# Kernel tuning notes

Measured on AMD Instinct MI355X. Metric: run time of the kernel, lower is better.

The kernel has to match this reference:

```python
import jax, jax.numpy as jnp
import numpy as np

B, N, TOKEN_DIM = 8, 1024, 768
H, D = 12, 64  # n_heads, head_dim


def setup_inputs() -> dict:
    key = jax.random.key(0)
    k1, k2, k3, k4 = jax.random.split(key, 4)
    x = jax.random.normal(k1, (B, N, TOKEN_DIM), dtype=jnp.float32)
    # nn.Linear(token_dim, 3*H*D, bias=False); store as (in, out)
    W_qkv = jax.random.normal(k2, (TOKEN_DIM, 3 * H * D), dtype=jnp.float32) * (TOKEN_DIM ** -0.5)
    # nn.Linear(H*D, token_dim) with bias
    W_out = jax.random.normal(k3, (H * D, TOKEN_DIM), dtype=jnp.float32) * ((H * D) ** -0.5)
    b_out = jax.random.normal(k4, (TOKEN_DIM,), dtype=jnp.float32) * 0.01
    return {"x": x, "W_qkv": W_qkv, "W_out": W_out, "b_out": b_out}


def reference(x, W_qkv, W_out, b_out):
    b, n, _ = x.shape
    qkv = x @ W_qkv                              # (B, N, 3*H*D)
    # Faithful to original: reshape directly to (B, 3, H, N, D)
    qkv = qkv.reshape(b, 3, H, n, D)
    q, k, v = qkv[:, 0], qkv[:, 1], qkv[:, 2]    # each (B, H, N, D)
    scale = D ** -0.5
    scores = jnp.einsum('bhnd,bhmd->bhnm', q, k) * scale
    probs = jax.nn.softmax(scores, axis=-1)
    attn = jnp.einsum('bhnm,bhmd->bhnd', probs, v)  # (B, H, N, D)
    attn = attn.transpose(0, 2, 1, 3).reshape(b, n, H * D)
    out = attn @ W_out + b_out                    # dropout p=0.0 is identity
    return out
```

## Files before the change

### kernel.cpp

```cpp
#include <hip/hip_runtime.h>
#include <math.h>

static constexpr int NB   = 8;
static constexpr int SEQ  = 1024;
static constexpr int TD   = 768;
static constexpr int NH   = 12;
static constexpr int HD   = 64;
static constexpr int QKVC = 3 * NH * HD;

static constexpr size_t BATCH_ELEMS = (size_t)SEQ * QKVC;
static constexpr size_t THIRD_ELEMS = (size_t)NH * SEQ * HD;
static constexpr size_t HEAD_ELEMS  = (size_t)SEQ * HD;

typedef __bf16 bf16x8 __attribute__((ext_vector_type(8)));
typedef __bf16 bf16x4 __attribute__((ext_vector_type(4)));
typedef float  f32x4  __attribute__((ext_vector_type(4)));

#define MFMA16(a, b, c) __builtin_amdgcn_mfma_f32_16x16x32_bf16((a), (b), (c), 0, 0, 0)

static constexpr float SCL2E = 0.18033688011112042f;

__device__ __forceinline__ void gload_lds16(const void* g, void* l) {
  __builtin_amdgcn_global_load_lds(
      (const __attribute__((address_space(1))) unsigned int*)g,
      (__attribute__((address_space(3))) unsigned int*)l, 16, 0, 0);
}

__global__ __launch_bounds__(256) void cast_f32_bf16(const float* __restrict__ in,
                                                     __bf16* __restrict__ out, int n4) {
  int i = blockIdx.x * 256 + threadIdx.x;
  if (i < n4) {
    float4 v = ((const float4*)in)[i];
    bf16x4 o;
    o[0] = (__bf16)v.x; o[1] = (__bf16)v.y; o[2] = (__bf16)v.z; o[3] = (__bf16)v.w;
    ((bf16x4*)out)[i] = o;
  }
}

__global__ __launch_bounds__(256) void wtrans(const float* __restrict__ W,
                                              __bf16* __restrict__ Wt, int K, int N) {
  __shared__ float T[32 * 33];
  const int tid = threadIdx.x;
  const int k0 = blockIdx.y * 32, n0 = blockIdx.x * 32;
#pragma unroll
  for (int i = 0; i < 4; ++i) {
    int idx = tid + i * 256;
    int kk = idx >> 5, nn = idx & 31;
    T[kk * 33 + nn] = W[(size_t)(k0 + kk) * N + n0 + nn];
  }
  __syncthreads();
#pragma unroll
  for (int i = 0; i < 4; ++i) {
    int idx = tid + i * 256;
    int nn = idx >> 5, kk = idx & 31;
    Wt[(size_t)(n0 + nn) * K + k0 + kk] = (__bf16)T[kk * 33 + nn];
  }
}

__global__ __launch_bounds__(256) void vtrans(const __bf16* __restrict__ qkvb,
                                              __bf16* __restrict__ vtb) {
  const int nt = blockIdx.x;
  const int h = blockIdx.y;
  const int b = blockIdx.z;
  __shared__ __bf16 T[128 * 72];
  const int tid = threadIdx.x;
  const int n0 = nt * 128;
  const __bf16* Vb = qkvb + (size_t)b * BATCH_ELEMS + 2 * THIRD_ELEMS + (size_t)h * HEAD_ELEMS;
#pragma unroll
  for (int i = 0; i < 4; ++i) {
    int ch = tid + i * 256;
    int row = ch >> 3, c8 = ch & 7;
    *(bf16x8*)&T[row * 72 + c8 * 8] = *(const bf16x8*)&Vb[(size_t)(n0 + row) * HD + c8 * 8];
  }
  __syncthreads();
#pragma unroll
  for (int i = 0; i < 4; ++i) {
    int ch = tid + i * 256;
    int d = ch >> 4, n8 = ch & 15;
    bf16x8 v;
#pragma unroll
    for (int jj = 0; jj < 8; ++jj) {
      int j = (jj + n8) & 7;
      v[j] = T[(n8 * 8 + j) * 72 + d];
    }
    *(bf16x8*)&vtb[((size_t)((b * NH + h) * HD) + d) * SEQ + n0 + n8 * 8] = v;
  }
}

template <int MODE, int BM>
__global__ __launch_bounds__(256) void gemm_mfma(const __bf16* __restrict__ A,
                                                 const __bf16* __restrict__ Bt,
                                                 const float* __restrict__ bias,
                                                 void* __restrict__ C,
                                                 int M, int N, int K) {
  constexpr int MI = BM / 32;
  __shared__ __bf16 As[2][BM * 32];
  __shared__ __bf16 Bs[2][128 * 32];
  const int tid = threadIdx.x;
  const int lane = tid & 63;
  const int wid = tid >> 6;
  const int wr = wid >> 1, wc = wid & 1;
  const int r = lane & 15, g = lane >> 4;
  const size_t bm = (size_t)blockIdx.y * BM;
  const size_t bn = (size_t)blockIdx.x * 128;

  const int srow = lane >> 2;
  const int scol = (lane & 3) * 8;

  auto stage = [&](int buf, int k0) {
#pragma unroll
    for (int j = 0; j < BM / 64; ++j) {
      const int rowbase = wid * (BM / 4) + j * 16;
      gload_lds16(&A[(bm + rowbase + srow) * K + k0 + scol], &As[buf][rowbase * 32]);
    }
#pragma unroll
    for (int j = 0; j < 2; ++j) {
      const int rowbase = wid * 32 + j * 16;
      gload_lds16(&Bt[(bn + rowbase + srow) * K + k0 + scol], &Bs[buf][rowbase * 32]);
    }
  };

  f32x4 acc[MI][4];
#pragma unroll
  for (int mi = 0; mi < MI; ++mi)
#pragma unroll
    for (int nj = 0; nj < 4; ++nj) acc[mi][nj] = (f32x4){0.f, 0.f, 0.f, 0.f};

  stage(0, 0);
  __syncthreads();

  int cur = 0;
  for (int k0 = 0; k0 < K; k0 += 32) {
    if (k0 + 32 < K) stage(cur ^ 1, k0 + 32);
    bf16x8 af[MI], bf[4];
#pragma unroll
    for (int mi = 0; mi < MI; ++mi)
      af[mi] = *(const bf16x8*)&As[cur][(wr * (BM / 2) + mi * 16 + r) * 32 + g * 8];
#pragma unroll
    for (int nj = 0; nj < 4; ++nj)
      bf[nj] = *(const bf16x8*)&Bs[cur][(wc * 64 + nj * 16 + r) * 32 + g * 8];
    __builtin_amdgcn_s_setprio(1);
#pragma unroll
    for (int mi = 0; mi < MI; ++mi)
#pragma unroll
      for (int nj = 0; nj < 4; ++nj)
        acc[mi][nj] = MFMA16(af[mi], bf[nj], acc[mi][nj]);
    __builtin_amdgcn_s_setprio(0);
    __syncthreads();
    cur ^= 1;
  }

  const int orow0 = g * 4;
  const int ocol = r;
#pragma unroll
  for (int mi = 0; mi < MI; ++mi)
#pragma unroll
    for (int nj = 0; nj < 4; ++nj)
#pragma unroll
      for (int reg = 0; reg < 4; ++reg) {
        size_t rrow = bm + wr * (BM / 2) + mi * 16 + orow0 + reg;
        size_t ccol = bn + wc * 64 + nj * 16 + ocol;
        float v = acc[mi][nj][reg];
        if (MODE == 1) {
          int fwb = ((int)(rrow & (SEQ - 1))) * QKVC + (int)ccol;
          float vv = (fwb < (int)THIRD_ELEMS) ? v * SCL2E : v;
          ((__bf16*)C)[rrow * N + ccol] = (__bf16)vv;
        } else {
          ((float*)C)[rrow * N + ccol] = v + bias[ccol];
        }
      }
}

__global__ __launch_bounds__(256) void attn_mfma(const __bf16* __restrict__ qkvb,
                                                 const __bf16* __restrict__ vtb,
                                                 __bf16* __restrict__ attn2b) {
  const int d = blockIdx.x;
  const int qt = (d >> 3) & 7;
  const int hb = (d >> 6) * 8 + (d & 7);
  const int b = hb / NH, h = hb % NH;

  const int tid = threadIdx.x;
  const int lane = tid & 63;
  const int w = tid >> 6;
  const int c = lane & 15, g = lane >> 4;

  __shared__ __bf16 KsF[2][4096];
  __shared__ __bf16 VsF[2][4096];

  const __bf16* Qb = qkvb + (size_t)b * BATCH_ELEMS + (size_t)h * HEAD_ELEMS;
  const __bf16* Kb = Qb + THIRD_ELEMS;
  const __bf16* Vtb = vtb + (size_t)((b * NH + h) * HD) * SEQ;

  const __bf16* kS[2];
  const __bf16* vS[2];
  int ldsOff[2];
#pragma unroll
  for (int i = 0; i < 2; ++i) {
    const int t2f = i * 4 + w;
    const int t = t2f >> 1, f = t2f & 1;
    const int krow = ((t >> 1) << 5) | ((c >> 2) << 3) | ((t & 1) << 2) | (c & 3);
    kS[i] = Kb + krow * HD + f * 32 + g * 8;
    const int db = t2f >> 1, kk = t2f & 1;
    vS[i] = Vtb + (db * 16 + c) * SEQ + kk * 32 + g * 8;
    ldsOff[i] = t2f * 512;
  }

  bf16x8 qf[2][2];
#pragma unroll
  for (int s = 0; s < 2; ++s) {
    const int q0s = qt * 128 + s * 64 + w * 16;
#pragma unroll
    for (int f = 0; f < 2; ++f)
      qf[s][f] = *(const bf16x8*)&Qb[(size_t)(q0s + c) * HD + f * 32 + g * 8];
  }

  f32x4 Oa[2][4];
#pragma unroll
  for (int s = 0; s < 2; ++s)
#pragma unroll
    for (int db = 0; db < 4; ++db) Oa[s][db] = (f32x4){0.f, 0.f, 0.f, 0.f};
  float lpart[2] = {0.f, 0.f};

#pragma unroll
  for (int i = 0; i < 2; ++i) {
    gload_lds16(kS[i], &KsF[0][ldsOff[i]]);
    gload_lds16(vS[i], &VsF[0][ldsOff[i]]);
    kS[i] += 64 * HD;
    vS[i] += 64;
  }
  __syncthreads();

  int cur = 0;
  for (int it = 0; it < SEQ / 64; ++it) {
    if (it < SEQ / 64 - 1) {
      const int nxt = cur ^ 1;
#pragma unroll
      for (int i = 0; i < 2; ++i) {
        gload_lds16(kS[i], &KsF[nxt][ldsOff[i]]);
        gload_lds16(vS[i], &VsF[nxt][ldsOff[i]]);
        kS[i] += 64 * HD;
        vS[i] += 64;
      }
    }

    f32x4 sa[2][4];
#pragma unroll
    for (int s = 0; s < 2; ++s)
#pragma unroll
      for (int t = 0; t < 4; ++t) sa[s][t] = (f32x4){0.f, 0.f, 0.f, 0.f};
    __builtin_amdgcn_s_setprio(1);
#pragma unroll
    for (int t = 0; t < 4; ++t)
#pragma unroll
      for (int f = 0; f < 2; ++f) {
        bf16x8 kf = *(const bf16x8*)&KsF[cur][(t * 2 + f) * 512 + lane * 8];
        sa[0][t] = MFMA16(kf, qf[0][f], sa[0][t]);
        sa[1][t] = MFMA16(kf, qf[1][f], sa[1][t]);
      }
    __builtin_amdgcn_s_setprio(0);

    bf16x8 pb[2][2];
#pragma unroll
    for (int s = 0; s < 2; ++s) {
      float p[4][4];
      float lp = 0.f;
#pragma unroll
      for (int t = 0; t < 4; ++t)
#pragma unroll
        for (int reg = 0; reg < 4; ++reg) {
          float pv = __builtin_exp2f(sa[s][t][reg]);
          p[t][reg] = pv;
          lp += pv;
        }
      lpart[s] += lp;
#pragma unroll
      for (int kk = 0; kk < 2; ++kk)
#pragma unroll
        for (int i = 0; i < 4; ++i) {
          pb[s][kk][i] = (__bf16)p[2 * kk][i];
          pb[s][kk][4 + i] = (__bf16)p[2 * kk + 1][i];
        }
    }

    __builtin_amdgcn_s_setprio(1);
#pragma unroll
    for (int db = 0; db < 4; ++db)
#pragma unroll
      for (int kk = 0; kk < 2; ++kk) {
        bf16x8 vf = *(const bf16x8*)&VsF[cur][(db * 2 + kk) * 512 + lane * 8];
        Oa[0][db] = MFMA16(vf, pb[0][kk], Oa[0][db]);
        Oa[1][db] = MFMA16(vf, pb[1][kk], Oa[1][db]);
      }
    __builtin_amdgcn_s_setprio(0);

    __syncthreads();
    cur ^= 1;
  }

#pragma unroll
  for (int s = 0; s < 2; ++s) {
    float lrow = lpart[s];
    lrow += __shfl_xor(lrow, 16);
    lrow += __shfl_xor(lrow, 32);
    const float inv = 1.0f / lrow;
    const size_t rowq = (size_t)(b * SEQ) + qt * 128 + s * 64 + w * 16 + c;
#pragma unroll
    for (int db = 0; db < 4; ++db) {
      bf16x4 o;
#pragma unroll
      for (int reg = 0; reg < 4; ++reg) o[reg] = (__bf16)(Oa[s][db][reg] * inv);
      *(bf16x4*)&attn2b[rowq * TD + h * HD + db * 16 + g * 4] = o;
    }
  }
}

extern "C" void kernel_launch(void* const* d_in, const int* in_sizes, int n_in,
                              void* d_out, int out_size, void* d_ws,
                              size_t ws_size, hipStream_t stream) {
  const float* x = (const float*)d_in[0];
  const float* W_qkv = (const float*)d_in[1];
  const float* W_out = (const float*)d_in[2];
  const float* b_out = (const float*)d_in[3];
  float* out = (float*)d_out;

  __bf16* xb = (__bf16*)d_ws;
  __bf16* wqkvt = xb + (size_t)NB * SEQ * TD;
  __bf16* woutt = wqkvt + (size_t)QKVC * TD;
  __bf16* qkvb = woutt + (size_t)TD * TD;
  __bf16* vtb = qkvb + (size_t)NB * SEQ * QKVC;
  __bf16* attn2b = vtb + (size_t)NB * NH * HD * SEQ;

  cast_f32_bf16<<<(NB * SEQ * TD / 4 + 255) / 256, 256, 0, stream>>>(x, xb, NB * SEQ * TD / 4);
  wtrans<<<dim3(QKVC / 32, TD / 32), 256, 0, stream>>>(W_qkv, wqkvt, TD, QKVC);
  wtrans<<<dim3(TD / 32, TD / 32), 256, 0, stream>>>(W_out, woutt, TD, TD);

  gemm_mfma<1, 128><<<dim3(QKVC / 128, NB * SEQ / 128), 256, 0, stream>>>(
      xb, wqkvt, nullptr, qkvb, NB * SEQ, QKVC, TD);

  vtrans<<<dim3(SEQ / 128, NH, NB), 256, 0, stream>>>(qkvb, vtb);

  attn_mfma<<<dim3(SEQ / 128 * NH * NB), 256, 0, stream>>>(qkvb, vtb, attn2b);

  gemm_mfma<0, 64><<<dim3(TD / 128, NB * SEQ / 64), 256, 0, stream>>>(
      attn2b, woutt, b_out, out, NB * SEQ, TD, TD);
}
```

Baseline: 153.3 us.

## Load attention K/V fragments directly from global into registers, drop LDS staging

The attention kernel no longer stages K and V tiles through double-buffered shared memory with async global-to-LDS loads and per-iteration barriers. Each wave now loads its MFMA fragments for K and V straight from global memory into registers every iteration, and the loop is kept rolled. The setprio hints around MFMA blocks are also removed in both the GEMM and attention kernels. This removes LDS traffic and __syncthreads, but every wave now re-reads the same K/V data from global/L2 and loses the prefetch overlap, so it depends on cache hits and latency hiding.

```diff
diff --git a/kernel.cpp b/kernel.cpp
--- a/kernel.cpp
+++ b/kernel.cpp
@@ -139,13 +139,11 @@
 #pragma unroll
     for (int nj = 0; nj < 4; ++nj)
       bf[nj] = *(const bf16x8*)&Bs[cur][(wc * 64 + nj * 16 + r) * 32 + g * 8];
-    __builtin_amdgcn_s_setprio(1);
 #pragma unroll
     for (int mi = 0; mi < MI; ++mi)
 #pragma unroll
       for (int nj = 0; nj < 4; ++nj)
         acc[mi][nj] = MFMA16(af[mi], bf[nj], acc[mi][nj]);
-    __builtin_amdgcn_s_setprio(0);
     __syncthreads();
     cur ^= 1;
   }
@@ -184,26 +182,16 @@
   const int w = tid >> 6;
   const int c = lane & 15, g = lane >> 4;
 
-  __shared__ __bf16 KsF[2][4096];
-  __shared__ __bf16 VsF[2][4096];
-
   const __bf16* Qb = qkvb + (size_t)b * BATCH_ELEMS + (size_t)h * HEAD_ELEMS;
   const __bf16* Kb = Qb + THIRD_ELEMS;
   const __bf16* Vtb = vtb + (size_t)((b * NH + h) * HD) * SEQ;
 
-  const __bf16* kS[2];
-  const __bf16* vS[2];
-  int ldsOff[2];
-#pragma unroll
-  for (int i = 0; i < 2; ++i) {
-    const int t2f = i * 4 + w;
-    const int t = t2f >> 1, f = t2f & 1;
-    const int krow = ((t >> 1) << 5) | ((c >> 2) << 3) | ((t & 1) << 2) | (c & 3);
-    kS[i] = Kb + krow * HD + f * 32 + g * 8;
-    const int db = t2f >> 1, kk = t2f & 1;
-    vS[i] = Vtb + (db * 16 + c) * SEQ + kk * 32 + g * 8;
-    ldsOff[i] = t2f * 512;
-  }
+  const __bf16* kb0 = Kb + ((c >> 2) * 8 + (c & 3)) * HD + g * 8;
+  const __bf16* kb1 = kb0 + 2048;
+  const __bf16* vb0 = Vtb + (size_t)(0 * 16 + c) * SEQ + g * 8;
+  const __bf16* vb1 = Vtb + (size_t)(1 * 16 + c) * SEQ + g * 8;
+  const __bf16* vb2 = Vtb + (size_t)(2 * 16 + c) * SEQ + g * 8;
+  const __bf16* vb3 = Vtb + (size_t)(3 * 16 + c) * SEQ + g * 8;
 
   bf16x8 qf[2][2];
 #pragma unroll
@@ -221,26 +209,23 @@
     for (int db = 0; db < 4; ++db) Oa[s][db] = (f32x4){0.f, 0.f, 0.f, 0.f};
   float lpart[2] = {0.f, 0.f};
 
-#pragma unroll
-  for (int i = 0; i < 2; ++i) {
-    gload_lds16(kS[i], &KsF[0][ldsOff[i]]);
-    gload_lds16(vS[i], &VsF[0][ldsOff[i]]);
-    kS[i] += 64 * HD;
-    vS[i] += 64;
-  }
-  __syncthreads();
-
-  int cur = 0;
+#pragma unroll 1
   for (int it = 0; it < SEQ / 64; ++it) {
-    if (it < SEQ / 64 - 1) {
-      const int nxt = cur ^ 1;
-#pragma unroll
-      for (int i = 0; i < 2; ++i) {
-        gload_lds16(kS[i], &KsF[nxt][ldsOff[i]]);
-        gload_lds16(vS[i], &VsF[nxt][ldsOff[i]]);
-        kS[i] += 64 * HD;
-        vS[i] += 64;
+    bf16x8 kfr[4][2];
+#pragma unroll
+    for (int tt = 0; tt < 2; ++tt)
+#pragma unroll
+      for (int f = 0; f < 2; ++f) {
+        kfr[tt][f] = *(const bf16x8*)(kb0 + tt * 256 + f * 32);
+        kfr[tt + 2][f] = *(const bf16x8*)(kb1 + tt * 256 + f * 32);
       }
+    bf16x8 vfr[4][2];
+#pragma unroll
+    for (int kk = 0; kk < 2; ++kk) {
+      vfr[0][kk] = *(const bf16x8*)(vb0 + kk * 32);
+      vfr[1][kk] = *(const bf16x8*)(vb1 + kk * 32);
+      vfr[2][kk] = *(const bf16x8*)(vb2 + kk * 32);
+      vfr[3][kk] = *(const bf16x8*)(vb3 + kk * 32);
     }
 
     f32x4 sa[2][4];
@@ -248,16 +233,13 @@
     for (int s = 0; s < 2; ++s)
 #pragma unroll
       for (int t = 0; t < 4; ++t) sa[s][t] = (f32x4){0.f, 0.f, 0.f, 0.f};
-    __builtin_amdgcn_s_setprio(1);
 #pragma unroll
     for (int t = 0; t < 4; ++t)
 #pragma unroll
       for (int f = 0; f < 2; ++f) {
-        bf16x8 kf = *(const bf16x8*)&KsF[cur][(t * 2 + f) * 512 + lane * 8];
-        sa[0][t] = MFMA16(kf, qf[0][f], sa[0][t]);
-        sa[1][t] = MFMA16(kf, qf[1][f], sa[1][t]);
+        sa[0][t] = MFMA16(kfr[t][f], qf[0][f], sa[0][t]);
+        sa[1][t] = MFMA16(kfr[t][f], qf[1][f], sa[1][t]);
       }
-    __builtin_amdgcn_s_setprio(0);
 
     bf16x8 pb[2][2];
 #pragma unroll
@@ -282,19 +264,20 @@
         }
     }
 
-    __builtin_amdgcn_s_setprio(1);
 #pragma unroll
     for (int db = 0; db < 4; ++db)
 #pragma unroll
       for (int kk = 0; kk < 2; ++kk) {
-        bf16x8 vf = *(const bf16x8*)&VsF[cur][(db * 2 + kk) * 512 + lane * 8];
-        Oa[0][db] = MFMA16(vf, pb[0][kk], Oa[0][db]);
-        Oa[1][db] = MFMA16(vf, pb[1][kk], Oa[1][db]);
+        Oa[0][db] = MFMA16(vfr[db][kk], pb[0][kk], Oa[0][db]);
+        Oa[1][db] = MFMA16(vfr[db][kk], pb[1][kk], Oa[1][db]);
       }
-    __builtin_amdgcn_s_setprio(0);
-
-    __syncthreads();
-    cur ^= 1;
+
+    kb0 += 64 * HD;
+    kb1 += 64 * HD;
+    vb0 += 64;
+    vb1 += 64;
+    vb2 += 64;
+    vb3 += 64;
   }
 
 #pragma unroll
```

After: 185.0 us. 20.6% more time.
